# Kernel tuning notes

Hardware: AMD Instinct MI355X
Metric: run time of the kernel (lower is better)

## Reference

```python
import jax, jax.numpy as jnp
import numpy as np

B, S, H, E = 32, 4096, 512, 512
NEG = -1000000000.0


def setup_inputs() -> dict:
    key = jax.random.key(0)
    ks = jax.random.split(key, 8)
    query = jax.random.normal(ks[0], (B, H), dtype=jnp.float32)
    keys = jax.random.normal(ks[1], (B, S, E), dtype=jnp.float32)
    mask = jax.random.randint(ks[2], (B, S), 0, 2, dtype=jnp.int32)
    # learned params (torch Linear: y = x @ W.T + b); store W already transposed
    Wq = jax.random.normal(ks[3], (H, H), dtype=jnp.float32) / np.sqrt(H)
    bq = jnp.zeros((H,), dtype=jnp.float32)
    Wk = jax.random.normal(ks[4], (E, H), dtype=jnp.float32) / np.sqrt(E)
    bk = jnp.zeros((H,), dtype=jnp.float32)
    v = jax.random.normal(ks[5], (H,), dtype=jnp.float32) / np.sqrt(H)
    bv = jnp.zeros((), dtype=jnp.float32)
    return {"query": query, "keys": keys, "mask": mask,
            "Wq": Wq, "bq": bq, "Wk": Wk, "bk": bk, "v": v, "bv": bv}


def reference(query, keys, mask, Wq, bq, Wk, bk, v, bv):
    # q_proj: (B, 1, H); k_proj: (B, S, H)
    q_proj = (query @ Wq + bq)[:, None, :]
    k_proj = jnp.einsum('bse,eh->bsh', keys, Wk) + bk
    # additive score: v^T tanh(q + k) + bv -> (B, S)
    scores = jnp.einsum('bsh,h->bs', jnp.tanh(q_proj + k_proj), v) + bv
    scores = jnp.where(mask == 0, NEG, scores)
    attn = jax.nn.softmax(scores, axis=-1)          # (B, S)
    context = jnp.einsum('bs,bse->be', attn, keys)  # (B, E)
    return context, attn
```

## Files before the change

kernel.cpp:

```cpp
#include <hip/hip_runtime.h>
#include <hip/hip_bf16.h>

#define BB 32
#define SS 4096
#define HH 512
#define EE 512
#define NCH 64
#define NEGV -1000000000.0f

using float4v = __attribute__((ext_vector_type(4))) float;
using short8v = __attribute__((ext_vector_type(8))) short;

#if defined(__has_builtin)
#if __has_builtin(__builtin_amdgcn_sched_barrier)
#define SCHED_FENCE() __builtin_amdgcn_sched_barrier(0)
#endif
#if __has_builtin(__builtin_amdgcn_rcpf)
#define FAST_RCP(x) __builtin_amdgcn_rcpf(x)
#endif
#if __has_builtin(__builtin_amdgcn_s_setprio)
#define SETPRIO(n) __builtin_amdgcn_s_setprio(n)
#endif
#endif
#ifndef SCHED_FENCE
#define SCHED_FENCE()
#endif
#ifndef FAST_RCP
#define FAST_RCP(x) (1.0f / (x))
#endif
#ifndef SETPRIO
#define SETPRIO(n)
#endif

__device__ inline unsigned short f2bf(float x) {
    union { float f; unsigned int u; } c; c.f = x;
    unsigned int r = c.u + 0x7FFFu + ((c.u >> 16) & 1u);
    return (unsigned short)(r >> 16);
}
__device__ inline float bf2f(unsigned short s) {
    union { float f; unsigned int u; } c; c.u = ((unsigned int)s) << 16;
    return c.f;
}
__device__ inline unsigned int pk2bf(float a, float b) {
    union { __hip_bfloat162 h; unsigned int u; } c;
    c.h = __float22bfloat162_rn(float2{a, b});
    return c.u;
}

__global__ void prep_kernel(const float* __restrict__ query, const float* __restrict__ Wq,
                            float* __restrict__ qp4,
                            const float* __restrict__ Wk, unsigned short* __restrict__ WkT) {
    int bx = blockIdx.x, t = threadIdx.x;
    if (bx < 4 * BB) {
        __shared__ float qs[128];
        int b = bx >> 2, seg = bx & 3;
        if (t < 128) qs[t] = query[b * HH + seg * 128 + t];
        __syncthreads();
        float a0 = 0.f, a1 = 0.f;
        const float* wq = Wq + (size_t)(seg * 128) * HH;
        #pragma unroll 8
        for (int e = 0; e < 128; ++e) {
            float q = qs[e];
            a0 += q * wq[(size_t)e * HH + t];
            a1 += q * wq[(size_t)e * HH + t + 256];
        }
        qp4[((size_t)seg * BB + b) * HH + t] = a0;
        qp4[((size_t)seg * BB + b) * HH + t + 256] = a1;
    } else {
        int g = (bx - 4 * BB) * 256 + t;
        int lane = g & 63, nt = (g >> 6) & 31, ks = g >> 11;
        int lq = lane >> 4, lr = lane & 15;
        int h = nt * 16 + lr;
        int e0 = ks * 32 + lq * 8;
        short8v o;
        #pragma unroll
        for (int j = 0; j < 8; ++j) o[j] = (short)f2bf(Wk[(size_t)(e0 + j) * HH + h]);
        *(short8v*)(WkT + (size_t)g * 8) = o;
    }
}

__launch_bounds__(512, 4)
__global__ void fused_kernel(const float* __restrict__ keys, const unsigned short* __restrict__ WkT,
                             const float* __restrict__ qp4, const float* __restrict__ bq,
                             const float* __restrict__ bk, const float* __restrict__ v,
                             const float* __restrict__ bv, const int* __restrict__ mask,
                             float* __restrict__ pe_out, float* __restrict__ part,
                             float* __restrict__ marr, float* __restrict__ larr) {
    constexpr int LDK = EE + 8;
    __shared__ unsigned short klds[64 * LDK];
    __shared__ float qp_lds[HH];
    __shared__ float v_lds[HH];
    __shared__ float red[8][64];
    __shared__ float p_lds[64];
    int b = blockIdx.y, c = blockIdx.x, s0 = c * 64;
    int tid = threadIdx.x;

    const float4v* ksrc = (const float4v*)(keys + ((size_t)b * SS + s0) * EE);
    float4v kv[4];
    #pragma unroll
    for (int p = 0; p < 4; ++p) {
        int idx = tid + p * 512;
        kv[p] = ksrc[(size_t)(idx >> 5) * 128 + (idx & 31)];
    }
    int mval = 0;
    if (tid < 64) mval = mask[b * SS + s0 + tid];

    for (int i = tid; i < HH; i += 512) {
        qp_lds[i] = qp4[((size_t)0 * BB + b) * HH + i] + qp4[((size_t)1 * BB + b) * HH + i]
                  + qp4[((size_t)2 * BB + b) * HH + i] + qp4[((size_t)3 * BB + b) * HH + i]
                  + bq[i] + bk[i];
        v_lds[i] = v[i];
    }

    #pragma unroll
    for (int p = 0; p < 4; ++p) {
        int idx = tid + p * 512, row = idx >> 5, c4 = idx & 31;
        unsigned int u0 = pk2bf(kv[p].x, kv[p].y), u1 = pk2bf(kv[p].z, kv[p].w);
        *(uint2*)(&klds[row * LDK + c4 * 4]) = make_uint2(u0, u1);
    }

    int w = tid >> 6, lane = tid & 63;
    int lq = lane >> 4, lr = lane & 15;
    int nt0 = w * 4;
    const short8v* Wf = (const short8v*)WkT;

    short8v bcur[4];
    #pragma unroll
    for (int j = 0; j < 4; ++j) bcur[j] = Wf[(size_t)(nt0 + j) * 64 + lane];

    float4v acc[4][4];
    #pragma unroll
    for (int m = 0; m < 4; ++m)
        #pragma unroll
        for (int j = 0; j < 4; ++j) acc[m][j] = (float4v){0.f, 0.f, 0.f, 0.f};

    __syncthreads();

    #pragma unroll
    for (int q = 0; q < 4; ++q) {
        if (q < 3) {
            #pragma unroll
            for (int p = 0; p < 4; ++p) {
                int idx = tid + p * 512;
                kv[p] = ksrc[(size_t)(idx >> 5) * 128 + (q + 1) * 32 + (idx & 31)];
            }
        }
        SCHED_FENCE();
        #pragma unroll
        for (int ksl = 0; ksl < 4; ++ksl) {
            int kq = q * 4 + ksl;
            short8v bn[4];
            if (kq < 15) {
                #pragma unroll
                for (int j = 0; j < 4; ++j)
                    bn[j] = Wf[((size_t)(kq + 1) * 32 + nt0 + j) * 64 + lane];
            }
            SETPRIO(1);
            #pragma unroll
            for (int m = 0; m < 4; ++m) {
                short8v afrag = *(const short8v*)(&klds[(m * 16 + lr) * LDK + kq * 32 + lq * 8]);
                #pragma unroll
                for (int j = 0; j < 4; ++j)
                    acc[m][j] = __builtin_amdgcn_mfma_f32_16x16x32_bf16(afrag, bcur[j], acc[m][j], 0, 0, 0);
            }
            SETPRIO(0);
            if (kq < 15) {
                #pragma unroll
                for (int j = 0; j < 4; ++j) bcur[j] = bn[j];
            }
        }
        if (q < 3) {
            #pragma unroll
            for (int p = 0; p < 4; ++p) {
                int idx = tid + p * 512, row = idx >> 5, c4 = (q + 1) * 32 + (idx & 31);
                unsigned int u0 = pk2bf(kv[p].x, kv[p].y), u1 = pk2bf(kv[p].z, kv[p].w);
                *(uint2*)(&klds[row * LDK + c4 * 4]) = make_uint2(u0, u1);
            }
            __syncthreads();
        }
    }

    float part_r[4][4];
    #pragma unroll
    for (int m = 0; m < 4; ++m)
        #pragma unroll
        for (int r = 0; r < 4; ++r) part_r[m][r] = 0.f;
    #pragma unroll
    for (int j = 0; j < 4; ++j) {
        int h = (nt0 + j) * 16 + lr;
        float vj = v_lds[h], qj = qp_lds[h], vj2 = -2.f * vj;
        #pragma unroll
        for (int m = 0; m < 4; ++m) {
            #pragma unroll
            for (int r = 0; r < 4; ++r) {
                float x = qj + acc[m][j][r];
                float rr = FAST_RCP(__expf(x + x) + 1.f);
                part_r[m][r] += __builtin_fmaf(vj2, rr, vj);
            }
        }
    }
    #pragma unroll
    for (int m = 0; m < 4; ++m)
        #pragma unroll
        for (int r = 0; r < 4; ++r) {
            float p = part_r[m][r];
            p += __shfl_xor(p, 1, 16);
            p += __shfl_xor(p, 2, 16);
            p += __shfl_xor(p, 4, 16);
            p += __shfl_xor(p, 8, 16);
            part_r[m][r] = p;
        }
    if (lr == 0) {
        #pragma unroll
        for (int m = 0; m < 4; ++m)
            #pragma unroll
            for (int r = 0; r < 4; ++r)
                red[w][m * 16 + lq * 4 + r] = part_r[m][r];
    }
    __syncthreads();

    if (tid < 64) {
        float sc = red[0][tid] + red[1][tid] + red[2][tid] + red[3][tid]
                 + red[4][tid] + red[5][tid] + red[6][tid] + red[7][tid] + bv[0];
        if (mval == 0) sc = NEGV;
        float mv = sc;
        #pragma unroll
        for (int off = 1; off < 64; off <<= 1) mv = fmaxf(mv, __shfl_xor(mv, off));
        float pe = __expf(sc - mv);
        float ls = pe;
        #pragma unroll
        for (int off = 1; off < 64; off <<= 1) ls += __shfl_xor(ls, off);
        p_lds[tid] = pe;
        pe_out[b * SS + s0 + tid] = pe;
        if (tid == 0) { marr[b * NCH + c] = mv; larr[b * NCH + c] = ls; }
    }
    __syncthreads();

    {
        float o0 = 0.f, o1 = 0.f;
        #pragma unroll 8
        for (int s = 0; s < 32; ++s) {
            o0 += p_lds[s]      * bf2f(klds[s * LDK + tid]);
            o1 += p_lds[s + 32] * bf2f(klds[(s + 32) * LDK + tid]);
        }
        part[((size_t)b * NCH + c) * EE + tid] = o0 + o1;
    }
}

__global__ void finalize_kernel(const float* __restrict__ pe_arr, const float* __restrict__ part,
                                const float* __restrict__ marr, const float* __restrict__ larr,
                                float* __restrict__ ctx, float* __restrict__ attn) {
    __shared__ float wgt[NCH];
    __shared__ float Ls;
    int b = blockIdx.y, px = blockIdx.x, t = threadIdx.x;
    if (t < NCH) {
        float m = marr[b * NCH + t], l = larr[b * NCH + t];
        float M = m;
        #pragma unroll
        for (int off = 1; off < 64; off <<= 1) M = fmaxf(M, __shfl_xor(M, off));
        float wq = __expf(m - M);
        float L = wq * l;
        #pragma unroll
        for (int off = 1; off < 64; off <<= 1) L += __shfl_xor(L, off);
        wgt[t] = wq;
        if (t == 0) Ls = L;
    }
    __syncthreads();
    float invL = 1.f / Ls;
    if (px == 0) {
        float o = 0.f;
        #pragma unroll 8
        for (int cc = 0; cc < NCH; ++cc)
            o += wgt[cc] * part[((size_t)b * NCH + cc) * EE + t];
        ctx[b * EE + t] = o * invL;
    }
    int s0 = px * 1024;
    attn[b * SS + s0 + t]       = pe_arr[b * SS + s0 + t]       * wgt[(s0 + t) >> 6]       * invL;
    attn[b * SS + s0 + t + 512] = pe_arr[b * SS + s0 + t + 512] * wgt[(s0 + t + 512) >> 6] * invL;
}

extern "C" void kernel_launch(void* const* d_in, const int* in_sizes, int n_in,
                              void* d_out, int out_size, void* d_ws, size_t ws_size,
                              hipStream_t stream) {
    const float* query = (const float*)d_in[0];
    const float* keys  = (const float*)d_in[1];
    const int*   mask  = (const int*)d_in[2];
    const float* Wq    = (const float*)d_in[3];
    const float* bq    = (const float*)d_in[4];
    const float* Wk    = (const float*)d_in[5];
    const float* bk    = (const float*)d_in[6];
    const float* v     = (const float*)d_in[7];
    const float* bv    = (const float*)d_in[8];

    float* out  = (float*)d_out;
    float* ctx  = out;
    float* attn = out + BB * EE;

    char* ws = (char*)d_ws;
    float* qp4          = (float*)ws;
    unsigned short* WkT = (unsigned short*)(ws + 262144);
    float* pe           = (float*)(ws + 786432);
    float* part         = (float*)(ws + 1310720);
    float* marr         = (float*)(ws + 5505024);
    float* larr         = (float*)(ws + 5513216);

    prep_kernel<<<256, 256, 0, stream>>>(query, Wq, qp4, Wk, WkT);
    fused_kernel<<<dim3(NCH, BB), 512, 0, stream>>>(keys, WkT, qp4, bq, bk, v, bv, mask,
                                                    pe, part, marr, larr);
    finalize_kernel<<<dim3(4, BB), 512, 0, stream>>>(pe, part, marr, larr, ctx, attn);
}
```

Measured before the change: 414.3 us.

## Split query projection finer, tile WkT transpose, interleave LDS fill, exp2 tanh

```diff
diff --git a/kernel.cpp b/kernel.cpp
--- a/kernel.cpp
+++ b/kernel.cpp
@@ -6,6 +6,7 @@
 #define HH 512
 #define EE 512
 #define NCH 64
+#define QSEG 8
 #define NEGV -1000000000.0f
 
 using float4v = __attribute__((ext_vector_type(4))) float;
@@ -18,6 +19,9 @@
 #if __has_builtin(__builtin_amdgcn_rcpf)
 #define FAST_RCP(x) __builtin_amdgcn_rcpf(x)
 #endif
+#if __has_builtin(__builtin_amdgcn_exp2f)
+#define FAST_EXP2(x) __builtin_amdgcn_exp2f(x)
+#endif
 #if __has_builtin(__builtin_amdgcn_s_setprio)
 #define SETPRIO(n) __builtin_amdgcn_s_setprio(n)
 #endif
@@ -27,6 +31,9 @@
 #endif
 #ifndef FAST_RCP
 #define FAST_RCP(x) (1.0f / (x))
+#endif
+#ifndef FAST_EXP2
+#define FAST_EXP2(x) __expf(0.69314718056f * (x))
 #endif
 #ifndef SETPRIO
 #define SETPRIO(n)
@@ -48,40 +55,53 @@
 }
 
 __global__ void prep_kernel(const float* __restrict__ query, const float* __restrict__ Wq,
-                            float* __restrict__ qp4,
+                            float* __restrict__ qp8,
                             const float* __restrict__ Wk, unsigned short* __restrict__ WkT) {
     int bx = blockIdx.x, t = threadIdx.x;
-    if (bx < 4 * BB) {
-        __shared__ float qs[128];
-        int b = bx >> 2, seg = bx & 3;
-        if (t < 128) qs[t] = query[b * HH + seg * 128 + t];
+    if (bx < QSEG * BB) {
+        __shared__ float qs[64];
+        int b = bx >> 3, seg = bx & 7;
+        if (t < 64) qs[t] = query[b * HH + seg * 64 + t];
         __syncthreads();
         float a0 = 0.f, a1 = 0.f;
-        const float* wq = Wq + (size_t)(seg * 128) * HH;
+        const float* wq = Wq + (size_t)(seg * 64) * HH;
         #pragma unroll 8
-        for (int e = 0; e < 128; ++e) {
+        for (int e = 0; e < 64; ++e) {
             float q = qs[e];
             a0 += q * wq[(size_t)e * HH + t];
             a1 += q * wq[(size_t)e * HH + t + 256];
         }
-        qp4[((size_t)seg * BB + b) * HH + t] = a0;
-        qp4[((size_t)seg * BB + b) * HH + t + 256] = a1;
+        qp8[((size_t)seg * BB + b) * HH + t] = a0;
+        qp8[((size_t)seg * BB + b) * HH + t + 256] = a1;
     } else {
-        int g = (bx - 4 * BB) * 256 + t;
-        int lane = g & 63, nt = (g >> 6) & 31, ks = g >> 11;
+        int tile = bx - QSEG * BB;
+        int ks = tile >> 3;
+        int h0 = (tile & 7) * 64;
+        __shared__ float wt[32][67];
+        #pragma unroll
+        for (int p = 0; p < 2; ++p) {
+            int idx = t + p * 256;
+            int r = idx >> 4, c4 = idx & 15;
+            float4v wv = *(const float4v*)(Wk + (size_t)(ks * 32 + r) * HH + h0 + c4 * 4);
+            wt[r][c4 * 4 + 0] = wv.x; wt[r][c4 * 4 + 1] = wv.y;
+            wt[r][c4 * 4 + 2] = wv.z; wt[r][c4 * 4 + 3] = wv.w;
+        }
+        __syncthreads();
+        int lane = t & 63, ntl = t >> 6;
         int lq = lane >> 4, lr = lane & 15;
-        int h = nt * 16 + lr;
-        int e0 = ks * 32 + lq * 8;
+        int nt = (h0 >> 4) + ntl;
         short8v o;
         #pragma unroll
-        for (int j = 0; j < 8; ++j) o[j] = (short)f2bf(Wk[(size_t)(e0 + j) * HH + h]);
-        *(short8v*)(WkT + (size_t)g * 8) = o;
+        for (int j = 0; j < 8; ++j)
+            o[j] = (short)f2bf(wt[lq * 8 + j][ntl * 16 + lr]);
+        size_t g = ((size_t)ks * 32 + nt) * 64 + lane;
+        *(short8v*)(WkT + g * 8) = o;
     }
 }
 
 __launch_bounds__(512, 4)
 __global__ void fused_kernel(const float* __restrict__ keys, const unsigned short* __restrict__ WkT,
-                             const float* __restrict__ qp4, const float* __restrict__ bq,
+                             const float* __restrict__ qp8, const float* __restrict__ bq,
                              const float* __restrict__ bk, const float* __restrict__ v,
                              const float* __restrict__ bv, const int* __restrict__ mask,
                              float* __restrict__ pe_out, float* __restrict__ part,
@@ -92,6 +112,7 @@
     __shared__ float v_lds[HH];
     __shared__ float red[8][64];
     __shared__ float p_lds[64];
+    __shared__ float ctxred[2][EE];
     int b = blockIdx.y, c = blockIdx.x, s0 = c * 64;
     int tid = threadIdx.x;
 
@@ -106,9 +127,10 @@
     if (tid < 64) mval = mask[b * SS + s0 + tid];
 
     for (int i = tid; i < HH; i += 512) {
-        qp_lds[i] = qp4[((size_t)0 * BB + b) * HH + i] + qp4[((size_t)1 * BB + b) * HH + i]
-                  + qp4[((size_t)2 * BB + b) * HH + i] + qp4[((size_t)3 * BB + b) * HH + i]
-                  + bq[i] + bk[i];
+        float qv = 0.f;
+        #pragma unroll
+        for (int sg = 0; sg < QSEG; ++sg) qv += qp8[((size_t)sg * BB + b) * HH + i];
+        qp_lds[i] = qv + bq[i] + bk[i];
         v_lds[i] = v[i];
     }
 
@@ -168,16 +190,16 @@
                 #pragma unroll
                 for (int j = 0; j < 4; ++j) bcur[j] = bn[j];
             }
-        }
-        if (q < 3) {
-            #pragma unroll
-            for (int p = 0; p < 4; ++p) {
-                int idx = tid + p * 512, row = idx >> 5, c4 = (q + 1) * 32 + (idx & 31);
-                unsigned int u0 = pk2bf(kv[p].x, kv[p].y), u1 = pk2bf(kv[p].z, kv[p].w);
-                *(uint2*)(&klds[row * LDK + c4 * 4]) = make_uint2(u0, u1);
-            }
-            __syncthreads();
-        }
+            if (ksl == 2 && q < 3) {
+                #pragma unroll
+                for (int p = 0; p < 4; ++p) {
+                    int idx = tid + p * 512, row = idx >> 5, c4 = (q + 1) * 32 + (idx & 31);
+                    unsigned int u0 = pk2bf(kv[p].x, kv[p].y), u1 = pk2bf(kv[p].z, kv[p].w);
+                    *(uint2*)(&klds[row * LDK + c4 * 4]) = make_uint2(u0, u1);
+                }
+            }
+        }
+        if (q < 3) __syncthreads();
     }
 
     float part_r[4][4];
@@ -194,7 +216,7 @@
             #pragma unroll
             for (int r = 0; r < 4; ++r) {
                 float x = qj + acc[m][j][r];
-                float rr = FAST_RCP(__expf(x + x) + 1.f);
+                float rr = FAST_RCP(FAST_EXP2(2.885390082f * x) + 1.f);
                 part_r[m][r] += __builtin_fmaf(vj2, rr, vj);
             }
         }
@@ -237,14 +259,20 @@
     __syncthreads();
 
     {
-        float o0 = 0.f, o1 = 0.f;
+        int c2 = (tid & 255) * 2;
+        int sb = (tid >> 8) * 32;
+        float e0 = 0.f, e1 = 0.f;
         #pragma unroll 8
         for (int s = 0; s < 32; ++s) {
-            o0 += p_lds[s]      * bf2f(klds[s * LDK + tid]);
-            o1 += p_lds[s + 32] * bf2f(klds[(s + 32) * LDK + tid]);
-        }
-        part[((size_t)b * NCH + c) * EE + tid] = o0 + o1;
-    }
+            unsigned int u = *(const unsigned int*)(&klds[(sb + s) * LDK + c2]);
+            float ps = p_lds[sb + s];
+            e0 = __builtin_fmaf(ps, bf2f((unsigned short)(u & 0xffffu)), e0);
+            e1 = __builtin_fmaf(ps, bf2f((unsigned short)(u >> 16)), e1);
+        }
+        *(float2*)(&ctxred[tid >> 8][c2]) = make_float2(e0, e1);
+    }
+    __syncthreads();
+    part[((size_t)b * NCH + c) * EE + tid] = ctxred[0][tid] + ctxred[1][tid];
 }
 
 __global__ void finalize_kernel(const float* __restrict__ pe_arr, const float* __restrict__ part,
@@ -297,15 +325,15 @@
     float* attn = out + BB * EE;
 
     char* ws = (char*)d_ws;
-    float* qp4          = (float*)ws;
-    unsigned short* WkT = (unsigned short*)(ws + 262144);
-    float* pe           = (float*)(ws + 786432);
-    float* part         = (float*)(ws + 1310720);
-    float* marr         = (float*)(ws + 5505024);
-    float* larr         = (float*)(ws + 5513216);
-
-    prep_kernel<<<256, 256, 0, stream>>>(query, Wq, qp4, Wk, WkT);
-    fused_kernel<<<dim3(NCH, BB), 512, 0, stream>>>(keys, WkT, qp4, bq, bk, v, bv, mask,
+    float* qp8          = (float*)ws;
+    unsigned short* WkT = (unsigned short*)(ws + 524288);
+    float* pe           = (float*)(ws + 1048576);
+    float* part         = (float*)(ws + 1572864);
+    float* marr         = (float*)(ws + 5767168);
+    float* larr         = (float*)(ws + 5775360);
+
+    prep_kernel<<<QSEG * BB + 128, 256, 0, stream>>>(query, Wq, qp8, Wk, WkT);
+    fused_kernel<<<dim3(NCH, BB), 512, 0, stream>>>(keys, WkT, qp8, bq, bk, v, bv, mask,
                                                     pe, part, marr, larr);
     finalize_kernel<<<dim3(4, BB), 512, 0, stream>>>(pe, part, marr, larr, ctx, attn);
 }
```

Result: slower. 456.6 us (+10.2%).
